# Performance work log

Measured on AMD Instinct MI355X. Metric: run time of the kernel, lower is better.

The kernel has to match this reference:

```python
import jax, jax.numpy as jnp
import numpy as np

B, T, N, H, RC, APT = 8, 32, 144, 16, 16, 10
HN = H * N          # 2304
RCN = RC * N        # 2304
NUM_LAYERS = 2


def _lstm_scan(x, Wih, Whh, bih, bhh):
    # x: [B, D, T] -> hidden states [B, HN, T]; matches torch.nn.LSTMCell math
    b = x.shape[0]
    hd = Whh.shape[1]
    xs = jnp.moveaxis(x, 2, 0)  # [T, B, D]

    def step(carry, xt):
        h, c = carry
        g = xt @ Wih.T + bih + h @ Whh.T + bhh  # [B, 4*HN]
        i, f, gg, o = jnp.split(g, 4, axis=1)
        c = jax.nn.sigmoid(f) * c + jax.nn.sigmoid(i) * jnp.tanh(gg)
        h = jax.nn.sigmoid(o) * jnp.tanh(c)
        return (h, c), h

    init = (jnp.zeros((b, hd), x.dtype), jnp.zeros((b, hd), x.dtype))
    _, hs = jax.lax.scan(step, init, xs)  # [T, B, HN]
    return jnp.moveaxis(hs, 0, 2)  # [B, HN, T]


def _graph_conv(x, A, Wg, bg):
    # x: [B, H, N, T]; diffusion order 2 over one adaptive support, then 1x1 conv
    x1 = jnp.einsum('bcvt,vw->bcwt', x, A)
    x2 = jnp.einsum('bcvt,vw->bcwt', x1, A)
    h = jnp.concatenate([x, x1, x2], axis=1)  # [B, 3H, N, T]
    return jnp.einsum('bcnt,oc->bont', h, Wg) + bg[None, :, None, None]


def _bn(x, g, b, eps=1e-5):
    # BatchNorm2d in training mode (batch statistics over N,H,W)
    m = x.mean(axis=(0, 2, 3), keepdims=True)
    v = x.var(axis=(0, 2, 3), keepdims=True)
    return g[None, :, None, None] * (x - m) * jax.lax.rsqrt(v + eps) + b[None, :, None, None]


def _forward(input_tensor, mask, input_tensor_bw, mask_bw, y, ymask,
             ws, bs, wc, bc, nodevec1, nodevec2,
             Wih_fw, Whh_fw, bih_fw, bhh_fw,
             Wih_bw, Whh_bw, bih_bw, bhh_bw,
             Wg, bg, gamma, beta,
             W_end1, b_end1, W_end2, b_end2,
             W_lo, b_lo, W_f1, b_f1, W_f2, b_f2):

    def feat(inp, m):
        # stack->transpose(2,3) then two 1x1 convs (in_channels=1 each), summed
        f1 = jnp.swapaxes(inp, 1, 2)[:, None]  # [B,1,N,T]
        f2 = jnp.swapaxes(m, 1, 2)[:, None]
        return (ws[None, :, None, None] * f1 + bs[None, :, None, None]
                + wc[None, :, None, None] * f2 + bc[None, :, None, None])

    x = feat(input_tensor, mask)          # [B, RC, N, T]
    x_bw = feat(input_tensor_bw, mask_bw)
    adp = jax.nn.softmax(jax.nn.relu(nodevec1 @ nodevec2), axis=1)  # [N, N]

    outputs = None
    for l in range(NUM_LAYERS):
        t_l = x.shape[3]
        hs = _lstm_scan(x.reshape(B, -1, t_l), Wih_fw[l], Whh_fw[l], bih_fw[l], bhh_fw[l])
        if l == 0:
            hs_bw = _lstm_scan(x_bw.reshape(B, -1, t_l), Wih_bw, Whh_bw, bih_bw, bhh_bw)
            hs = (hs + hs_bw[..., ::-1]) / 2.0
        gcn_in = jnp.tanh(hs.reshape(B, H, N, t_l))
        go = _graph_conv(gcn_in, adp, Wg[l], bg[l])  # [B, RC, N, t_l]
        outputs = go if outputs is None else go + outputs[..., -t_l:]
        x = _bn(go[..., ::2], gamma[l], beta[l])  # halve time dim

    out = jnp.einsum('bcnt,oc->bont', outputs, W_end1) + b_end1[None, :, None, None]
    out = jnp.einsum('bcnt,oc->bont', out, W_end2) + b_end2[None, :, None, None]
    out = jnp.einsum('bcnt,t->bcn', out, W_lo[0]) + b_lo[0]  # linear over time, squeeze
    out = jnp.concatenate([out, y, ymask], axis=-1)  # [B, T, 3N]
    out = out @ W_f1.T + b_f1
    out = out @ W_f2.T + b_f2
    return out  # [B, T, N]


def setup_inputs() -> dict:
    key = jax.random.key(0)
    ks = iter(jax.random.split(key, 48))
    nrm = lambda shape, s=0.05: jax.random.normal(next(ks), shape, dtype=jnp.float32) * s
    rnd = lambda shape: jax.random.uniform(next(ks), shape, dtype=jnp.float32)
    d = {}
    for name in ['input_tensor', 'mask', 'input_tensor_bw', 'mask_bw', 'y', 'ymask']:
        d[name] = rnd((B, T, N))
    d['ws'] = nrm((RC,), 0.2); d['bs'] = nrm((RC,))
    d['wc'] = nrm((RC,), 0.2); d['bc'] = nrm((RC,))
    d['nodevec1'] = nrm((N, APT), 1.0); d['nodevec2'] = nrm((APT, N), 1.0)
    d['Wih_fw'] = nrm((NUM_LAYERS, 4 * HN, RCN), 0.02)
    d['Whh_fw'] = nrm((NUM_LAYERS, 4 * HN, HN), 0.02)
    d['bih_fw'] = nrm((NUM_LAYERS, 4 * HN)); d['bhh_fw'] = nrm((NUM_LAYERS, 4 * HN))
    d['Wih_bw'] = nrm((4 * HN, RCN), 0.02); d['Whh_bw'] = nrm((4 * HN, HN), 0.02)
    d['bih_bw'] = nrm((4 * HN,)); d['bhh_bw'] = nrm((4 * HN,))
    d['Wg'] = nrm((NUM_LAYERS, RC, 3 * H), 0.1); d['bg'] = nrm((NUM_LAYERS, RC))
    d['gamma'] = jnp.ones((NUM_LAYERS, RC), jnp.float32)
    d['beta'] = jnp.zeros((NUM_LAYERS, RC), jnp.float32)
    d['W_end1'] = nrm((H, RC), 0.1); d['b_end1'] = nrm((H,))
    d['W_end2'] = nrm((T, H), 0.1); d['b_end2'] = nrm((T,))
    d['W_lo'] = nrm((1, T // 2), 0.1); d['b_lo'] = nrm((1,))
    d['W_f1'] = nrm((128, 3 * N), 0.05); d['b_f1'] = nrm((128,))
    d['W_f2'] = nrm((N, 128), 0.05); d['b_f2'] = nrm((N,))
    return d


def reference(input_tensor, mask, input_tensor_bw, mask_bw, y, ymask,
              ws, bs, wc, bc, nodevec1, nodevec2,
              Wih_fw, Whh_fw, bih_fw, bhh_fw,
              Wih_bw, Whh_bw, bih_bw, bhh_bw,
              Wg, bg, gamma, beta,
              W_end1, b_end1, W_end2, b_end2,
              W_lo, b_lo, W_f1, b_f1, W_f2, b_f2):
    return _forward(input_tensor, mask, input_tensor_bw, mask_bw, y, ymask,
                    ws, bs, wc, bc, nodevec1, nodevec2,
                    Wih_fw, Whh_fw, bih_fw, bhh_fw,
                    Wih_bw, Whh_bw, bih_bw, bhh_bw,
                    Wg, bg, gamma, beta,
                    W_end1, b_end1, W_end2, b_end2,
                    W_lo, b_lo, W_f1, b_f1, W_f2, b_f2)
```

## Files before the change

### kernel.cpp

```cpp
#include <hip/hip_runtime.h>
#include <cstdint>
#include <cstddef>

#define HN_ 2304
#define G4_ 9216

typedef __attribute__((ext_vector_type(8))) short v8s;
typedef __attribute__((ext_vector_type(4))) float v4f;

__device__ __forceinline__ unsigned short f2bf(float x) {
  union { float f; unsigned int i; } v; v.f = x;
  unsigned int r = (v.i + 0x7fffu + ((v.i >> 16) & 1u)) >> 16;
  return (unsigned short)r;
}

__global__ __launch_bounds__(256) void adp_kernel(const float* __restrict__ nv1,
                                                  const float* __restrict__ nv2,
                                                  float* __restrict__ adp) {
  int i = blockIdx.x;
  int j = threadIdx.x;
  __shared__ float sm[256];
  float r = 0.f, v = -1e30f;
  if (j < 144) {
    for (int k = 0; k < 10; ++k) r += nv1[i * 10 + k] * nv2[k * 144 + j];
    r = fmaxf(r, 0.f);
    v = r;
  }
  sm[j] = v; __syncthreads();
  for (int s = 128; s > 0; s >>= 1) { if (j < s) sm[j] = fmaxf(sm[j], sm[j + s]); __syncthreads(); }
  float mx = sm[0]; __syncthreads();
  float e = (j < 144) ? expf(r - mx) : 0.f;
  sm[j] = e; __syncthreads();
  for (int s = 128; s > 0; s >>= 1) { if (j < s) sm[j] += sm[j + s]; __syncthreads(); }
  float sum = sm[0];
  if (j < 144) adp[i * 144 + j] = e / sum;
}

__global__ __launch_bounds__(256)
void eff_weights(const float* __restrict__ WihF, const float* __restrict__ WihB,
                 const float* __restrict__ bihF, const float* __restrict__ bhhF,
                 const float* __restrict__ bihB, const float* __restrict__ bhhB,
                 const float* __restrict__ ws, const float* __restrict__ bs,
                 const float* __restrict__ wc, const float* __restrict__ bc,
                 unsigned short* __restrict__ Wpk, float* __restrict__ beff) {
  const int r = blockIdx.x, dir = blockIdx.y;
  const float* W = dir ? WihB : WihF;
  __shared__ float red[256];
  const int n = threadIdx.x;
  float spb = 0.f;
  if (n < 144) {
    float sws = 0.f, swc = 0.f;
    #pragma unroll
    for (int c = 0; c < 16; ++c) {
      float w = W[(size_t)r * HN_ + c * 144 + n];
      sws += w * ws[c];
      swc += w * wc[c];
      spb += w * (bs[c] + bc[c]);
    }
    const int rm = r % 2304;
    const int g = r / 2304;
    const int nt = rm >> 2, col = (rm & 3) * 4 + g;
    unsigned short* outp = Wpk + (size_t)dir * 2654208;
    int k = n;
    outp[((size_t)(nt * 9 + (k >> 5)) * 64 + ((k >> 3) & 3) * 16 + col) * 8 + (k & 7)] = f2bf(sws);
    k = 144 + n;
    outp[((size_t)(nt * 9 + (k >> 5)) * 64 + ((k >> 3) & 3) * 16 + col) * 8 + (k & 7)] = f2bf(swc);
  }
  red[n] = spb; __syncthreads();
  for (int s = 128; s > 0; s >>= 1) { if (n < s) red[n] += red[n + s]; __syncthreads(); }
  if (n == 0) {
    const float* bih = dir ? bihB : bihF;
    const float* bhh = dir ? bhhB : bhhF;
    beff[dir * G4_ + r] = red[0] + bih[r] + bhh[r];
  }
}

__global__ void build_acat_frag(const float* __restrict__ inF, const float* __restrict__ mF,
                                const float* __restrict__ inB, const float* __restrict__ mB,
                                unsigned short* __restrict__ out) {
  int idx = blockIdx.x * 256 + threadIdx.x;
  int lane = idx & 63;
  int ks = (idx >> 6) % 9;
  int mt = (idx / (64 * 9)) % 16;
  int dir = idx / (64 * 9 * 16);
  int m = mt * 16 + (lane & 15);
  int k = ks * 32 + (lane >> 4) * 8;
  int t = m >> 3, b = m & 7;
  const float* src; int kk = k;
  if (k < 144) src = dir ? inB : inF;
  else { src = dir ? mB : mF; kk = k - 144; }
  const float* p = src + ((size_t)b * 32 + t) * 144 + kk;
  v8s o;
  #pragma unroll
  for (int e = 0; e < 8; ++e) o[e] = (short)f2bf(p[e]);
  ((v8s*)out)[idx] = o;
}

__global__ void pack_whh(const float* __restrict__ W, unsigned short* __restrict__ out) {
  int idx = blockIdx.x * 256 + threadIdx.x;
  int lane = idx & 63;
  int ks = (idx >> 6) % 72;
  int nt = idx / (64 * 72);
  int col = lane & 15, q = lane >> 4;
  int r = (col & 3) * 2304 + nt * 4 + (col >> 2);
  int k = ks * 32 + q * 8;
  const float* src = W + (size_t)r * 2304 + k;
  float4 v0 = *(const float4*)src;
  float4 v1 = *(const float4*)(src + 4);
  v8s o;
  o[0] = (short)f2bf(v0.x); o[1] = (short)f2bf(v0.y);
  o[2] = (short)f2bf(v0.z); o[3] = (short)f2bf(v0.w);
  o[4] = (short)f2bf(v1.x); o[5] = (short)f2bf(v1.y);
  o[6] = (short)f2bf(v1.z); o[7] = (short)f2bf(v1.w);
  ((v8s*)out)[idx] = o;
}

__global__ __launch_bounds__(64)
void gemm_frag(const unsigned short* __restrict__ Apk, const unsigned short* __restrict__ Wpk,
               const float* __restrict__ b1, const float* __restrict__ b2,
               float* __restrict__ Gx, int nks) {
  const int lane = threadIdx.x;
  const int nt = blockIdx.x;
  const int mtb = blockIdx.y * 4;
  v4f acc[4] = {};
  const v8s* Bp = (const v8s*)Wpk + (size_t)nt * nks * 64;
  const v8s* Ap = (const v8s*)Apk;
  for (int ks = 0; ks < nks; ++ks) {
    v8s bf = Bp[ks * 64 + lane];
    #pragma unroll
    for (int mi = 0; mi < 4; ++mi) {
      v8s af = Ap[(size_t)((mtb + mi) * nks + ks) * 64 + lane];
      acc[mi] = __builtin_amdgcn_mfma_f32_16x16x32_bf16(af, bf, acc[mi], 0, 0, 0);
    }
  }
  const int col = lane & 15;
  const int jj = col >> 2, g = col & 3;
  const int rw = g * 2304 + nt * 4 + jj;
  float bsum = b1[rw] + (b2 ? b2[rw] : 0.f);
  #pragma unroll
  for (int mi = 0; mi < 4; ++mi)
    #pragma unroll
    for (int r = 0; r < 4; ++r) {
      int m = (mtb + mi) * 16 + (lane >> 4) * 4 + r;
      int t = m >> 3, b = m & 7;
      Gx[((size_t)t * 576 + nt) * 128 + col * 8 + b] = acc[mi][r] + bsum;
    }
}

__global__ __launch_bounds__(256)
void lstm_mfma(const unsigned short* __restrict__ Wpk0, const unsigned short* __restrict__ Wpk1,
               const float* __restrict__ Gx0, const float* __restrict__ Gx1,
               const unsigned short* __restrict__ hin0, const unsigned short* __restrict__ hin1,
               unsigned short* __restrict__ hout0, unsigned short* __restrict__ hout1,
               float* __restrict__ c0, float* __restrict__ c1,
               float* __restrict__ hs0, float* __restrict__ hs1,
               int t, int t_l) {
  const int dir = blockIdx.y;
  const unsigned short* Wpk = dir ? Wpk1 : Wpk0;
  const float* Gx = (dir ? Gx1 : Gx0) + (size_t)t * 73728;
  const unsigned short* hin = dir ? hin1 : hin0;
  unsigned short* hout = dir ? hout1 : hout0;
  float* cb = dir ? c1 : c0;
  float* hsout = dir ? hs1 : hs0;

  __shared__ unsigned short Ash[36864];
  for (int i = threadIdx.x; i < 4608; i += 256)
    ((float4*)Ash)[i] = ((const float4*)hin)[i];
  __syncthreads();

  const int lane = threadIdx.x & 63;
  const int wave = threadIdx.x >> 6;
  const int nt = blockIdx.x * 4 + wave;

  v4f acc = {0.f, 0.f, 0.f, 0.f};
  const v8s* Ap = (const v8s*)Ash;
  const v8s* Bp = (const v8s*)Wpk + (size_t)nt * 72 * 64;
  #pragma unroll 8
  for (int ks = 0; ks < 72; ++ks) {
    v8s af = Ap[ks * 64 + lane];
    v8s bf = Bp[ks * 64 + lane];
    acc = __builtin_amdgcn_mfma_f32_16x16x32_bf16(af, bf, acc, 0, 0, 0);
  }

  float vI[4], vF[4], vG[4], vO[4];
  #pragma unroll
  for (int r = 0; r < 4; ++r) {
    float a = acc[r];
    vI[r] = a;
    vF[r] = __shfl_xor(a, 1, 64);
    vG[r] = __shfl_xor(a, 2, 64);
    vO[r] = __shfl_xor(a, 3, 64);
  }
  const int col = lane & 15;
  if ((lane & 3) == 0 && lane < 32) {
    const int j = nt * 4 + (col >> 2);
    #pragma unroll
    for (int r = 0; r < 4; ++r) {
      const int b = (lane >> 4) * 4 + r;
      const float gi = vI[r] + Gx[(nt * 16 + col + 0) * 8 + b];
      const float gf = vF[r] + Gx[(nt * 16 + col + 1) * 8 + b];
      const float gg = vG[r] + Gx[(nt * 16 + col + 2) * 8 + b];
      const float go = vO[r] + Gx[(nt * 16 + col + 3) * 8 + b];
      const float si = 1.f / (1.f + expf(-gi));
      const float sf = 1.f / (1.f + expf(-gf));
      const float so = 1.f / (1.f + expf(-go));
      const float cn = sf * cb[b * HN_ + j] + si * tanhf(gg);
      const float hv = so * tanhf(cn);
      cb[b * HN_ + j] = cn;
      hsout[(size_t)(b * HN_ + j) * t_l + t] = hv;
      hout[((size_t)(j >> 5) * 64 + ((j >> 3) & 3) * 16 + b) * 8 + (j & 7)] = f2bf(hv);
    }
  }
}

__global__ void combine_tanh(const float* __restrict__ hsF, const float* __restrict__ hsB,
                             float* __restrict__ gin, int t_l, int total) {
  int idx = blockIdx.x * 256 + threadIdx.x;
  if (idx >= total) return;
  int t = idx % t_l;
  float v;
  if (hsB) v = 0.5f * (hsF[idx] + hsB[idx - t + (t_l - 1 - t)]);
  else v = hsF[idx];
  gin[idx] = tanhf(v);
}

__global__ void gc1(const float* __restrict__ in, const float* __restrict__ A,
                    float* __restrict__ out, int t_l, int total) {
  int idx = blockIdx.x * 256 + threadIdx.x;
  if (idx >= total) return;
  int t = idx % t_l;
  int w = (idx / t_l) % 144;
  int bc = idx / (t_l * 144);
  const float* src = in + (size_t)bc * 144 * t_l + t;
  float acc = 0.f;
  for (int v = 0; v < 144; ++v) acc += src[(size_t)v * t_l] * A[v * 144 + w];
  out[idx] = acc;
}

__global__ void gc_out(const float* __restrict__ g0, const float* __restrict__ g1,
                       const float* __restrict__ g2, const float* __restrict__ Wg,
                       const float* __restrict__ bg, const float* __restrict__ prev,
                       float* __restrict__ out, int t_l, int total) {
  int idx = blockIdx.x * 256 + threadIdx.x;
  if (idx >= total) return;
  int t = idx % t_l;
  int n = (idx / t_l) % 144;
  int o = (idx / (t_l * 144)) % 16;
  int b = idx / (t_l * 144 * 16);
  float acc = bg[o];
  size_t base = ((size_t)b * 16 * 144 + n) * t_l + t;
  #pragma unroll
  for (int c = 0; c < 16; ++c) {
    size_t s = base + (size_t)c * 144 * t_l;
    acc += Wg[o * 48 + c] * g0[s] + Wg[o * 48 + 16 + c] * g1[s] + Wg[o * 48 + 32 + c] * g2[s];
  }
  if (prev) acc += prev[((size_t)(b * 16 + o) * 144 + n) * 32 + 16 + t];
  out[idx] = acc;
}

__global__ __launch_bounds__(256)
void bn_xt(const float* __restrict__ go, const float* __restrict__ gamma,
           const float* __restrict__ beta, unsigned short* __restrict__ xbf) {
  int c = blockIdx.x;
  __shared__ float s1[256], s2[256];
  float sum = 0.f, sq = 0.f;
  for (int i = threadIdx.x; i < 18432; i += 256) {
    int b = i / 2304; int rem = i - b * 2304; int n = rem / 16; int tt = rem & 15;
    float v = go[((size_t)(b * 16 + c) * 144 + n) * 32 + 2 * tt];
    sum += v; sq += v * v;
  }
  s1[threadIdx.x] = sum; s2[threadIdx.x] = sq; __syncthreads();
  for (int s = 128; s > 0; s >>= 1) {
    if (threadIdx.x < s) { s1[threadIdx.x] += s1[threadIdx.x + s]; s2[threadIdx.x] += s2[threadIdx.x + s]; }
    __syncthreads();
  }
  float mean = s1[0] / 18432.f;
  float var = s2[0] / 18432.f - mean * mean;
  float rs = rsqrtf(var + 1e-5f);
  float scale = gamma[c] * rs, shift = beta[c] - mean * scale;
  for (int i = threadIdx.x; i < 18432; i += 256) {
    int b = i / 2304; int rem = i - b * 2304; int n = rem / 16; int tt = rem & 15;
    float v = go[((size_t)(b * 16 + c) * 144 + n) * 32 + 2 * tt];
    int m = tt * 8 + b;
    int k = c * 144 + n;
    size_t pos = ((size_t)((m >> 4) * 72 + (k >> 5)) * 64 + ((k >> 3) & 3) * 16 + (m & 15)) * 8 + (k & 7);
    xbf[pos] = f2bf(v * scale + shift);
  }
}

__global__ void e1_kernel(const float* __restrict__ in, const float* __restrict__ W,
                          const float* __restrict__ bias, float* __restrict__ out) {
  int idx = blockIdx.x * 256 + threadIdx.x;
  int tt = idx & 15;
  int n = (idx >> 4) % 144;
  int o = (idx / (16 * 144)) % 16;
  int b = idx / (16 * 144 * 16);
  float acc = bias[o];
  size_t base = ((size_t)b * 16 * 144 + n) * 16 + tt;
  #pragma unroll
  for (int c = 0; c < 16; ++c) acc += in[base + (size_t)c * 144 * 16] * W[o * 16 + c];
  out[idx] = acc;
}
__global__ void e2_kernel(const float* __restrict__ in, const float* __restrict__ W,
                          const float* __restrict__ bias, float* __restrict__ out) {
  int idx = blockIdx.x * 256 + threadIdx.x;
  int tt = idx & 15;
  int n = (idx >> 4) % 144;
  int o2 = (idx / (16 * 144)) % 32;
  int b = idx / (16 * 144 * 32);
  float acc = bias[o2];
  size_t base = ((size_t)b * 16 * 144 + n) * 16 + tt;
  #pragma unroll
  for (int o = 0; o < 16; ++o) acc += in[base + (size_t)o * 144 * 16] * W[o2 * 16 + o];
  out[idx] = acc;
}
__global__ void e3_kernel(const float* __restrict__ in, const float* __restrict__ Wlo,
                          const float* __restrict__ blo, float* __restrict__ out) {
  int idx = blockIdx.x * 256 + threadIdx.x;
  int n = idx % 144;
  int o2 = (idx / 144) % 32;
  int b = idx / (144 * 32);
  float acc = blo[0];
  size_t base = ((size_t)(b * 32 + o2) * 144 + n) * 16;
  #pragma unroll
  for (int tt = 0; tt < 16; ++tt) acc += in[base + tt] * Wlo[tt];
  out[idx] = acc;
}
__global__ void f1_kernel(const float* __restrict__ o3, const float* __restrict__ y,
                          const float* __restrict__ ym, const float* __restrict__ W,
                          const float* __restrict__ bias, float* __restrict__ out) {
  int idx = blockIdx.x * 256 + threadIdx.x;
  int k = idx & 127;
  int t = (idx >> 7) & 31;
  int b = idx >> 12;
  float acc = bias[k];
  size_t rb = (size_t)(b * 32 + t) * 144;
  const float* wr = W + k * 432;
  for (int n = 0; n < 144; ++n)
    acc += o3[rb + n] * wr[n] + y[rb + n] * wr[144 + n] + ym[rb + n] * wr[288 + n];
  out[idx] = acc;
}
__global__ void f2_kernel(const float* __restrict__ f1b, const float* __restrict__ W,
                          const float* __restrict__ bias, float* __restrict__ out) {
  int idx = blockIdx.x * 256 + threadIdx.x;
  int n = idx % 144;
  int t = (idx / 144) % 32;
  int b = idx / (144 * 32);
  float acc = bias[n];
  size_t fb = (size_t)(b * 32 + t) * 128;
  const float* wr = W + n * 128;
  #pragma unroll 4
  for (int k = 0; k < 128; ++k) acc += f1b[fb + k] * wr[k];
  out[idx] = acc;
}

extern "C" void kernel_launch(void* const* d_in, const int* in_sizes, int n_in,
                              void* d_out, int out_size, void* d_ws, size_t ws_size,
                              hipStream_t stream) {
  const float* input_tensor = (const float*)d_in[0];
  const float* mask_    = (const float*)d_in[1];
  const float* input_bw = (const float*)d_in[2];
  const float* mask_bw  = (const float*)d_in[3];
  const float* y_in     = (const float*)d_in[4];
  const float* ymask    = (const float*)d_in[5];
  const float* ws_p = (const float*)d_in[6];
  const float* bs_p = (const float*)d_in[7];
  const float* wc_p = (const float*)d_in[8];
  const float* bc_p = (const float*)d_in[9];
  const float* nv1 = (const float*)d_in[10];
  const float* nv2 = (const float*)d_in[11];
  const float* Wih_fw = (const float*)d_in[12];
  const float* Whh_fw = (const float*)d_in[13];
  const float* bih_fw = (const float*)d_in[14];
  const float* bhh_fw = (const float*)d_in[15];
  const float* Wih_bw = (const float*)d_in[16];
  const float* Whh_bw = (const float*)d_in[17];
  const float* bih_bw = (const float*)d_in[18];
  const float* bhh_bw = (const float*)d_in[19];
  const float* Wg   = (const float*)d_in[20];
  const float* bg   = (const float*)d_in[21];
  const float* gam  = (const float*)d_in[22];
  const float* bet  = (const float*)d_in[23];
  const float* W_end1 = (const float*)d_in[24];
  const float* b_end1 = (const float*)d_in[25];
  const float* W_end2 = (const float*)d_in[26];
  const float* b_end2 = (const float*)d_in[27];
  const float* W_lo = (const float*)d_in[28];
  const float* b_lo = (const float*)d_in[29];
  const float* W_f1 = (const float*)d_in[30];
  const float* b_f1 = (const float*)d_in[31];
  const float* W_f2 = (const float*)d_in[32];
  const float* b_f2 = (const float*)d_in[33];

  char* base = (char*)d_ws;
  size_t off = 0;
  auto alloc = [&](size_t bytes) -> char* {
    char* p = base + off;
    off += (bytes + 255) & ~(size_t)255;
    return p;
  };
  float* adp   = (float*)alloc(144 * 144 * 4);
  unsigned short* Weffpk = (unsigned short*)alloc((size_t)2 * 2654208 * 2);
  float* beff  = (float*)alloc(2 * G4_ * 4);
  unsigned short* acatf  = (unsigned short*)alloc((size_t)2 * 73728 * 2);
  float* GxF   = (float*)alloc((size_t)32 * 73728 * 4);
  float* GxB   = (float*)alloc((size_t)32 * 73728 * 4);
  char*  zreg  = alloc(6 * 147456 + 3 * 73728);
  float* hsF   = (float*)alloc((size_t)589824 * 4);
  float* hsB   = (float*)alloc((size_t)589824 * 4);
  float* hsL   = (float*)alloc((size_t)294912 * 4);
  float* gin   = (float*)alloc((size_t)589824 * 4);
  float* x1b   = (float*)alloc((size_t)589824 * 4);
  float* x2b   = (float*)alloc((size_t)589824 * 4);
  float* out0  = (float*)alloc((size_t)589824 * 4);
  float* out1  = (float*)alloc((size_t)294912 * 4);
  unsigned short* xbf = (unsigned short*)alloc((size_t)294912 * 2);
  float* tmp1  = (float*)alloc((size_t)294912 * 4);
  float* tmp2  = (float*)alloc((size_t)589824 * 4);
  float* out3  = (float*)alloc((size_t)36864 * 4);
  float* f1b   = (float*)alloc((size_t)32768 * 4);
  unsigned short* P0 = (unsigned short*)alloc((size_t)2654208 * 8 * 2);
  unsigned short* P1 = (unsigned short*)alloc((size_t)2654208 * 8 * 2);

  unsigned short* hbfF[2] = {(unsigned short*)zreg, (unsigned short*)(zreg + 147456)};
  unsigned short* hbfB[2] = {(unsigned short*)(zreg + 2 * 147456), (unsigned short*)(zreg + 3 * 147456)};
  unsigned short* hbfL[2] = {(unsigned short*)(zreg + 4 * 147456), (unsigned short*)(zreg + 5 * 147456)};
  float* cF = (float*)(zreg + 6 * 147456);
  float* cB = (float*)(zreg + 6 * 147456 + 73728);
  float* cL = (float*)(zreg + 6 * 147456 + 2 * 73728);

  hipMemsetAsync(zreg, 0, 6 * 147456 + 3 * 73728, stream);

  adp_kernel<<<144, 256, 0, stream>>>(nv1, nv2, adp);
  eff_weights<<<dim3(G4_, 2), 256, 0, stream>>>(Wih_fw, Wih_bw, bih_fw, bhh_fw, bih_bw, bhh_bw,
                                                ws_p, bs_p, wc_p, bc_p, Weffpk, beff);
  build_acat_frag<<<72, 256, 0, stream>>>(input_tensor, mask_, input_bw, mask_bw, acatf);
  gemm_frag<<<dim3(576, 4), 64, 0, stream>>>(acatf, Weffpk, beff, nullptr, GxF, 9);
  gemm_frag<<<dim3(576, 4), 64, 0, stream>>>(acatf + 73728, Weffpk + 2654208, beff + G4_, nullptr, GxB, 9);
  pack_whh<<<10368, 256, 0, stream>>>(Whh_fw, P0);
  pack_whh<<<10368, 256, 0, stream>>>(Whh_bw, P1);

  for (int t = 0; t < 32; ++t) {
    lstm_mfma<<<dim3(144, 2), 256, 0, stream>>>(
        P0, P1, GxF, GxB,
        hbfF[t & 1], hbfB[t & 1], hbfF[(t + 1) & 1], hbfB[(t + 1) & 1],
        cF, cB, hsF, hsB, t, 32);
  }

  combine_tanh<<<2304, 256, 0, stream>>>(hsF, hsB, gin, 32, 589824);
  gc1<<<2304, 256, 0, stream>>>(gin, adp, x1b, 32, 589824);
  gc1<<<2304, 256, 0, stream>>>(x1b, adp, x2b, 32, 589824);
  gc_out<<<2304, 256, 0, stream>>>(gin, x1b, x2b, Wg, bg, nullptr, out0, 32, 589824);
  bn_xt<<<16, 256, 0, stream>>>(out0, gam, bet, xbf);

  const size_t WL1_off = (size_t)G4_ * HN_;
  pack_whh<<<10368, 256, 0, stream>>>(Wih_fw + WL1_off, P1);
  gemm_frag<<<dim3(576, 2), 64, 0, stream>>>(xbf, P1, bih_fw + G4_, bhh_fw + G4_, GxF, 72);
  pack_whh<<<10368, 256, 0, stream>>>(Whh_fw + WL1_off, P0);

  for (int t = 0; t < 16; ++t) {
    lstm_mfma<<<dim3(144, 1), 256, 0, stream>>>(
        P0, P0, GxF, GxF,
        hbfL[t & 1], hbfL[t & 1], hbfL[(t + 1) & 1], hbfL[(t + 1) & 1],
        cL, cL, hsL, hsL, t, 16);
  }

  combine_tanh<<<1152, 256, 0, stream>>>(hsL, nullptr, gin, 16, 294912);
  gc1<<<1152, 256, 0, stream>>>(gin, adp, x1b, 16, 294912);
  gc1<<<1152, 256, 0, stream>>>(x1b, adp, x2b, 16, 294912);
  gc_out<<<1152, 256, 0, stream>>>(gin, x1b, x2b, Wg + 16 * 48, bg + 16, out0, out1, 16, 294912);

  e1_kernel<<<1152, 256, 0, stream>>>(out1, W_end1, b_end1, tmp1);
  e2_kernel<<<2304, 256, 0, stream>>>(tmp1, W_end2, b_end2, tmp2);
  e3_kernel<<<144, 256, 0, stream>>>(tmp2, W_lo, b_lo, out3);
  f1_kernel<<<128, 256, 0, stream>>>(out3, y_in, ymask, W_f1, b_f1, f1b);
  f2_kernel<<<144, 256, 0, stream>>>(f1b, W_f2, b_f2, (float*)d_out);
}
```

Measured before the change: 1.745 ms.

## Replace per-timestep LSTM launches with persistent cooperative scan kernel

```diff
diff --git a/kernel.cpp b/kernel.cpp
--- a/kernel.cpp
+++ b/kernel.cpp
@@ -1,6 +1,9 @@
 #include <hip/hip_runtime.h>
+#include <hip/hip_cooperative_groups.h>
 #include <cstdint>
 #include <cstddef>
+
+namespace cg = cooperative_groups;
 
 #define HN_ 2304
 #define G4_ 9216
@@ -147,69 +150,102 @@
     }
 }
 
-__global__ __launch_bounds__(256)
-void lstm_mfma(const unsigned short* __restrict__ Wpk0, const unsigned short* __restrict__ Wpk1,
+__global__ __launch_bounds__(256, 2)
+void lstm_scan(const unsigned short* __restrict__ Wpk0, const unsigned short* __restrict__ Wpk1,
                const float* __restrict__ Gx0, const float* __restrict__ Gx1,
-               const unsigned short* __restrict__ hin0, const unsigned short* __restrict__ hin1,
-               unsigned short* __restrict__ hout0, unsigned short* __restrict__ hout1,
-               float* __restrict__ c0, float* __restrict__ c1,
+               unsigned short* hbuf,
                float* __restrict__ hs0, float* __restrict__ hs1,
-               int t, int t_l) {
-  const int dir = blockIdx.y;
-  const unsigned short* Wpk = dir ? Wpk1 : Wpk0;
-  const float* Gx = (dir ? Gx1 : Gx0) + (size_t)t * 73728;
-  const unsigned short* hin = dir ? hin1 : hin0;
-  unsigned short* hout = dir ? hout1 : hout0;
-  float* cb = dir ? c1 : c0;
-  float* hsout = dir ? hs1 : hs0;
-
-  __shared__ unsigned short Ash[36864];
-  for (int i = threadIdx.x; i < 4608; i += 256)
-    ((float4*)Ash)[i] = ((const float4*)hin)[i];
-  __syncthreads();
+               int T, int blocksPerDir) {
+  cg::grid_group grid = cg::this_grid();
+  const int dir = blockIdx.x / blocksPerDir;
+  const int cidx = blockIdx.x - dir * blocksPerDir;
+  const unsigned short* __restrict__ Wpk = dir ? Wpk1 : Wpk0;
+  const float* __restrict__ Gxb = dir ? Gx1 : Gx0;
+  float* __restrict__ hsout = dir ? hs1 : hs0;
+  unsigned short* hb = hbuf + (size_t)dir * 2 * 18432;
 
   const int lane = threadIdx.x & 63;
   const int wave = threadIdx.x >> 6;
-  const int nt = blockIdx.x * 4 + wave;
-
-  v4f acc = {0.f, 0.f, 0.f, 0.f};
-  const v8s* Ap = (const v8s*)Ash;
-  const v8s* Bp = (const v8s*)Wpk + (size_t)nt * 72 * 64;
-  #pragma unroll 8
-  for (int ks = 0; ks < 72; ++ks) {
-    v8s af = Ap[ks * 64 + lane];
-    v8s bf = Bp[ks * 64 + lane];
-    acc = __builtin_amdgcn_mfma_f32_16x16x32_bf16(af, bf, acc, 0, 0, 0);
-  }
-
-  float vI[4], vF[4], vG[4], vO[4];
-  #pragma unroll
-  for (int r = 0; r < 4; ++r) {
-    float a = acc[r];
-    vI[r] = a;
-    vF[r] = __shfl_xor(a, 1, 64);
-    vG[r] = __shfl_xor(a, 2, 64);
-    vO[r] = __shfl_xor(a, 3, 64);
-  }
+  const int nt = cidx * 4 + wave;
+
+  __shared__ __align__(16) unsigned short Ash[18432];
+
+  const v8s* __restrict__ Bs = (const v8s*)Wpk + (size_t)nt * 72 * 64 + lane;
+
+  v8s wreg[36];
+  #pragma unroll
+  for (int k = 0; k < 36; ++k) wreg[k] = Bs[k * 64];
+
+  const int afoff = (lane >> 4) * 8 + (lane & 7);
   const int col = lane & 15;
-  if ((lane & 3) == 0 && lane < 32) {
-    const int j = nt * 4 + (col >> 2);
+  const int j = nt * 4 + (col >> 2);
+  const int brow = (lane >> 4) * 4;
+  const bool act = ((lane & 3) == 0) && (lane < 32);
+  float creg[4] = {0.f, 0.f, 0.f, 0.f};
+
+  for (int t = 0; t < T; ++t) {
+    const unsigned short* hcur = hb + (t & 1) * 18432;
+    unsigned short* hnxt = hb + ((t + 1) & 1) * 18432;
+
+    for (int i = threadIdx.x; i < 2304; i += 256)
+      ((float4*)Ash)[i] = ((const float4*)hcur)[i];
+    __syncthreads();
+
+    const v8s* Ap = (const v8s*)Ash;
+    v4f acc0 = {0.f, 0.f, 0.f, 0.f}, acc1 = {0.f, 0.f, 0.f, 0.f};
+
+    v8s bf[6], nb[6];
+    #pragma unroll
+    for (int u = 0; u < 6; ++u) bf[u] = Bs[(36 + u) * 64];
+
+    #pragma unroll
+    for (int k = 0; k < 36; ++k) {
+      v8s af = Ap[k * 32 + afoff];
+      acc0 = __builtin_amdgcn_mfma_f32_16x16x32_bf16(af, wreg[k], acc0, 0, 0, 0);
+    }
+    #pragma unroll
+    for (int c = 0; c < 6; ++c) {
+      #pragma unroll
+      for (int u = 0; u < 6; ++u) { if (c < 5) nb[u] = Bs[(42 + c * 6 + u) * 64]; }
+      #pragma unroll
+      for (int u = 0; u < 6; ++u) {
+        v8s af = Ap[(36 + c * 6 + u) * 32 + afoff];
+        acc1 = __builtin_amdgcn_mfma_f32_16x16x32_bf16(af, bf[u], acc1, 0, 0, 0);
+      }
+      #pragma unroll
+      for (int u = 0; u < 6; ++u) { if (c < 5) bf[u] = nb[u]; }
+    }
+
+    float vI[4], vF[4], vG[4], vO[4];
     #pragma unroll
     for (int r = 0; r < 4; ++r) {
-      const int b = (lane >> 4) * 4 + r;
-      const float gi = vI[r] + Gx[(nt * 16 + col + 0) * 8 + b];
-      const float gf = vF[r] + Gx[(nt * 16 + col + 1) * 8 + b];
-      const float gg = vG[r] + Gx[(nt * 16 + col + 2) * 8 + b];
-      const float go = vO[r] + Gx[(nt * 16 + col + 3) * 8 + b];
-      const float si = 1.f / (1.f + expf(-gi));
-      const float sf = 1.f / (1.f + expf(-gf));
-      const float so = 1.f / (1.f + expf(-go));
-      const float cn = sf * cb[b * HN_ + j] + si * tanhf(gg);
-      const float hv = so * tanhf(cn);
-      cb[b * HN_ + j] = cn;
-      hsout[(size_t)(b * HN_ + j) * t_l + t] = hv;
-      hout[((size_t)(j >> 5) * 64 + ((j >> 3) & 3) * 16 + b) * 8 + (j & 7)] = f2bf(hv);
-    }
+      float a = acc0[r] + acc1[r];
+      vI[r] = a;
+      vF[r] = __shfl_xor(a, 1, 64);
+      vG[r] = __shfl_xor(a, 2, 64);
+      vO[r] = __shfl_xor(a, 3, 64);
+    }
+    if (act) {
+      const float* Gx = Gxb + (size_t)t * 73728 + (size_t)(nt * 16 + col) * 8;
+      #pragma unroll
+      for (int r = 0; r < 4; ++r) {
+        const int b = brow + r;
+        const float gi = vI[r] + Gx[b];
+        const float gf = vF[r] + Gx[8 + b];
+        const float gg = vG[r] + Gx[16 + b];
+        const float go = vO[r] + Gx[24 + b];
+        const float si = 1.f / (1.f + expf(-gi));
+        const float sf = 1.f / (1.f + expf(-gf));
+        const float so = 1.f / (1.f + expf(-go));
+        const float cn = sf * creg[r] + si * tanhf(gg);
+        creg[r] = cn;
+        const float hv = so * tanhf(cn);
+        hsout[(size_t)(b * HN_ + j) * T + t] = hv;
+        hnxt[((j >> 5) * 32 + ((j >> 3) & 3) * 8 + b) * 8 + (j & 7)] = f2bf(hv);
+      }
+    }
+    __threadfence();
+    grid.sync();
   }
 }
 
@@ -405,7 +441,7 @@
   unsigned short* acatf  = (unsigned short*)alloc((size_t)2 * 73728 * 2);
   float* GxF   = (float*)alloc((size_t)32 * 73728 * 4);
   float* GxB   = (float*)alloc((size_t)32 * 73728 * 4);
-  char*  zreg  = alloc(6 * 147456 + 3 * 73728);
+  char*  hz    = alloc(147456 + 73728);
   float* hsF   = (float*)alloc((size_t)589824 * 4);
   float* hsB   = (float*)alloc((size_t)589824 * 4);
   float* hsL   = (float*)alloc((size_t)294912 * 4);
@@ -422,14 +458,10 @@
   unsigned short* P0 = (unsigned short*)alloc((size_t)2654208 * 8 * 2);
   unsigned short* P1 = (unsigned short*)alloc((size_t)2654208 * 8 * 2);
 
-  unsigned short* hbfF[2] = {(unsigned short*)zreg, (unsigned short*)(zreg + 147456)};
-  unsigned short* hbfB[2] = {(unsigned short*)(zreg + 2 * 147456), (unsigned short*)(zreg + 3 * 147456)};
-  unsigned short* hbfL[2] = {(unsigned short*)(zreg + 4 * 147456), (unsigned short*)(zreg + 5 * 147456)};
-  float* cF = (float*)(zreg + 6 * 147456);
-  float* cB = (float*)(zreg + 6 * 147456 + 73728);
-  float* cL = (float*)(zreg + 6 * 147456 + 2 * 73728);
-
-  hipMemsetAsync(zreg, 0, 6 * 147456 + 3 * 73728, stream);
+  unsigned short* hbuf0 = (unsigned short*)hz;
+  unsigned short* hbufL = (unsigned short*)(hz + 147456);
+
+  hipMemsetAsync(hz, 0, 147456 + 73728, stream);
 
   adp_kernel<<<144, 256, 0, stream>>>(nv1, nv2, adp);
   eff_weights<<<dim3(G4_, 2), 256, 0, stream>>>(Wih_fw, Wih_bw, bih_fw, bhh_fw, bih_bw, bhh_bw,
@@ -440,11 +472,14 @@
   pack_whh<<<10368, 256, 0, stream>>>(Whh_fw, P0);
   pack_whh<<<10368, 256, 0, stream>>>(Whh_bw, P1);
 
-  for (int t = 0; t < 32; ++t) {
-    lstm_mfma<<<dim3(144, 2), 256, 0, stream>>>(
-        P0, P1, GxF, GxB,
-        hbfF[t & 1], hbfB[t & 1], hbfF[(t + 1) & 1], hbfB[(t + 1) & 1],
-        cF, cB, hsF, hsB, t, 32);
+  {
+    const unsigned short* aW0 = P0; const unsigned short* aW1 = P1;
+    const float* aG0 = GxF; const float* aG1 = GxB;
+    unsigned short* ah = hbuf0;
+    float* ahs0 = hsF; float* ahs1 = hsB;
+    int aT = 32, aB = 144;
+    void* args[] = {&aW0, &aW1, &aG0, &aG1, &ah, &ahs0, &ahs1, &aT, &aB};
+    hipLaunchCooperativeKernel((void*)lstm_scan, dim3(288), dim3(256), args, 0, stream);
   }
 
   combine_tanh<<<2304, 256, 0, stream>>>(hsF, hsB, gin, 32, 589824);
@@ -458,11 +493,14 @@
   gemm_frag<<<dim3(576, 2), 64, 0, stream>>>(xbf, P1, bih_fw + G4_, bhh_fw + G4_, GxF, 72);
   pack_whh<<<10368, 256, 0, stream>>>(Whh_fw + WL1_off, P0);
 
-  for (int t = 0; t < 16; ++t) {
-    lstm_mfma<<<dim3(144, 1), 256, 0, stream>>>(
-        P0, P0, GxF, GxF,
-        hbfL[t & 1], hbfL[t & 1], hbfL[(t + 1) & 1], hbfL[(t + 1) & 1],
-        cL, cL, hsL, hsL, t, 16);
+  {
+    const unsigned short* aW0 = P0; const unsigned short* aW1 = P0;
+    const float* aG0 = GxF; const float* aG1 = GxF;
+    unsigned short* ah = hbufL;
+    float* ahs0 = hsL; float* ahs1 = hsL;
+    int aT = 16, aB = 144;
+    void* args[] = {&aW0, &aW1, &aG0, &aG1, &ah, &ahs0, &ahs1, &aT, &aB};
+    hipLaunchCooperativeKernel((void*)lstm_scan, dim3(144), dim3(256), args, 0, stream);
   }
 
   combine_tanh<<<1152, 256, 0, stream>>>(hsL, nullptr, gin, 16, 294912);
```

Result: slower. 3.874 ms (+122.0%).

## Split LSTM step K-reduction across waves and compact h layout to drop padding

Applied to the files above, without the earlier changes.

```diff
diff --git a/kernel.cpp b/kernel.cpp
--- a/kernel.cpp
+++ b/kernel.cpp
@@ -147,68 +147,76 @@
     }
 }
 
-__global__ __launch_bounds__(256)
-void lstm_mfma(const unsigned short* __restrict__ Wpk0, const unsigned short* __restrict__ Wpk1,
+__global__ __launch_bounds__(256, 4)
+void lstm_step(const unsigned short* __restrict__ Wpk0, const unsigned short* __restrict__ Wpk1,
                const float* __restrict__ Gx0, const float* __restrict__ Gx1,
                const unsigned short* __restrict__ hin0, const unsigned short* __restrict__ hin1,
                unsigned short* __restrict__ hout0, unsigned short* __restrict__ hout1,
                float* __restrict__ c0, float* __restrict__ c1,
                float* __restrict__ hs0, float* __restrict__ hs1,
-               int t, int t_l) {
+               int t, int T) {
   const int dir = blockIdx.y;
-  const unsigned short* Wpk = dir ? Wpk1 : Wpk0;
-  const float* Gx = (dir ? Gx1 : Gx0) + (size_t)t * 73728;
-  const unsigned short* hin = dir ? hin1 : hin0;
-  unsigned short* hout = dir ? hout1 : hout0;
-  float* cb = dir ? c1 : c0;
-  float* hsout = dir ? hs1 : hs0;
-
-  __shared__ unsigned short Ash[36864];
-  for (int i = threadIdx.x; i < 4608; i += 256)
-    ((float4*)Ash)[i] = ((const float4*)hin)[i];
-  __syncthreads();
+  const unsigned short* __restrict__ Wpk = dir ? Wpk1 : Wpk0;
+  const float* __restrict__ Gxb = dir ? Gx1 : Gx0;
+  const unsigned short* __restrict__ hin = dir ? hin1 : hin0;
+  unsigned short* __restrict__ hout = dir ? hout1 : hout0;
+  float* __restrict__ cb = dir ? c1 : c0;
+  float* __restrict__ hsout = dir ? hs1 : hs0;
 
   const int lane = threadIdx.x & 63;
   const int wave = threadIdx.x >> 6;
-  const int nt = blockIdx.x * 4 + wave;
+  const int nt = blockIdx.x;
+
+  const int afoff = (lane >> 4) * 8 + (lane & 7);
+  const v8s* __restrict__ Aq = (const v8s*)hin + (size_t)(wave * 18) * 32 + afoff;
+  const v8s* __restrict__ Bq = (const v8s*)Wpk + (size_t)nt * 72 * 64 + (size_t)(wave * 18) * 64 + lane;
 
   v4f acc = {0.f, 0.f, 0.f, 0.f};
-  const v8s* Ap = (const v8s*)Ash;
-  const v8s* Bp = (const v8s*)Wpk + (size_t)nt * 72 * 64;
-  #pragma unroll 8
-  for (int ks = 0; ks < 72; ++ks) {
-    v8s af = Ap[ks * 64 + lane];
-    v8s bf = Bp[ks * 64 + lane];
+  #pragma unroll
+  for (int k = 0; k < 18; ++k) {
+    v8s af = Aq[k * 32];
+    v8s bf = Bq[k * 64];
     acc = __builtin_amdgcn_mfma_f32_16x16x32_bf16(af, bf, acc, 0, 0, 0);
   }
 
-  float vI[4], vF[4], vG[4], vO[4];
-  #pragma unroll
-  for (int r = 0; r < 4; ++r) {
-    float a = acc[r];
-    vI[r] = a;
-    vF[r] = __shfl_xor(a, 1, 64);
-    vG[r] = __shfl_xor(a, 2, 64);
-    vO[r] = __shfl_xor(a, 3, 64);
-  }
-  const int col = lane & 15;
-  if ((lane & 3) == 0 && lane < 32) {
-    const int j = nt * 4 + (col >> 2);
+  __shared__ v4f red[3][64];
+  if (wave) red[wave - 1][lane] = acc;
+  __syncthreads();
+  if (wave == 0) {
+    acc += red[0][lane];
+    acc += red[1][lane];
+    acc += red[2][lane];
+
+    float vI[4], vF[4], vG[4], vO[4];
     #pragma unroll
     for (int r = 0; r < 4; ++r) {
-      const int b = (lane >> 4) * 4 + r;
-      const float gi = vI[r] + Gx[(nt * 16 + col + 0) * 8 + b];
-      const float gf = vF[r] + Gx[(nt * 16 + col + 1) * 8 + b];
-      const float gg = vG[r] + Gx[(nt * 16 + col + 2) * 8 + b];
-      const float go = vO[r] + Gx[(nt * 16 + col + 3) * 8 + b];
-      const float si = 1.f / (1.f + expf(-gi));
-      const float sf = 1.f / (1.f + expf(-gf));
-      const float so = 1.f / (1.f + expf(-go));
-      const float cn = sf * cb[b * HN_ + j] + si * tanhf(gg);
-      const float hv = so * tanhf(cn);
-      cb[b * HN_ + j] = cn;
-      hsout[(size_t)(b * HN_ + j) * t_l + t] = hv;
-      hout[((size_t)(j >> 5) * 64 + ((j >> 3) & 3) * 16 + b) * 8 + (j & 7)] = f2bf(hv);
+      float a = acc[r];
+      vI[r] = a;
+      vF[r] = __shfl_xor(a, 1, 64);
+      vG[r] = __shfl_xor(a, 2, 64);
+      vO[r] = __shfl_xor(a, 3, 64);
+    }
+    const int col = lane & 15;
+    if ((lane & 3) == 0 && lane < 32) {
+      const int j = nt * 4 + (col >> 2);
+      const int brow = (lane >> 4) * 4;
+      const float* Gx = Gxb + (size_t)t * 73728 + (size_t)(nt * 16 + col) * 8;
+      #pragma unroll
+      for (int r = 0; r < 4; ++r) {
+        const int b = brow + r;
+        const float gi = vI[r] + Gx[b];
+        const float gf = vF[r] + Gx[8 + b];
+        const float gg = vG[r] + Gx[16 + b];
+        const float go = vO[r] + Gx[24 + b];
+        const float si = 1.f / (1.f + expf(-gi));
+        const float sf = 1.f / (1.f + expf(-gf));
+        const float so = 1.f / (1.f + expf(-go));
+        const float cn = sf * cb[b * HN_ + j] + si * tanhf(gg);
+        cb[b * HN_ + j] = cn;
+        const float hv = so * tanhf(cn);
+        hsout[(size_t)(b * HN_ + j) * T + t] = hv;
+        hout[((j >> 5) * 32 + ((j >> 3) & 3) * 8 + b) * 8 + (j & 7)] = f2bf(hv);
+      }
     }
   }
 }
@@ -405,7 +413,7 @@
   unsigned short* acatf  = (unsigned short*)alloc((size_t)2 * 73728 * 2);
   float* GxF   = (float*)alloc((size_t)32 * 73728 * 4);
   float* GxB   = (float*)alloc((size_t)32 * 73728 * 4);
-  char*  zreg  = alloc(6 * 147456 + 3 * 73728);
+  char*  hz    = alloc(442368);
   float* hsF   = (float*)alloc((size_t)589824 * 4);
   float* hsB   = (float*)alloc((size_t)589824 * 4);
   float* hsL   = (float*)alloc((size_t)294912 * 4);
@@ -422,14 +430,14 @@
   unsigned short* P0 = (unsigned short*)alloc((size_t)2654208 * 8 * 2);
   unsigned short* P1 = (unsigned short*)alloc((size_t)2654208 * 8 * 2);
 
-  unsigned short* hbfF[2] = {(unsigned short*)zreg, (unsigned short*)(zreg + 147456)};
-  unsigned short* hbfB[2] = {(unsigned short*)(zreg + 2 * 147456), (unsigned short*)(zreg + 3 * 147456)};
-  unsigned short* hbfL[2] = {(unsigned short*)(zreg + 4 * 147456), (unsigned short*)(zreg + 5 * 147456)};
-  float* cF = (float*)(zreg + 6 * 147456);
-  float* cB = (float*)(zreg + 6 * 147456 + 73728);
-  float* cL = (float*)(zreg + 6 * 147456 + 2 * 73728);
-
-  hipMemsetAsync(zreg, 0, 6 * 147456 + 3 * 73728, stream);
+  unsigned short* hF[2] = {(unsigned short*)hz,            (unsigned short*)(hz + 36864)};
+  unsigned short* hB[2] = {(unsigned short*)(hz + 73728),  (unsigned short*)(hz + 110592)};
+  unsigned short* hL[2] = {(unsigned short*)(hz + 147456), (unsigned short*)(hz + 184320)};
+  float* cF = (float*)(hz + 221184);
+  float* cB = (float*)(hz + 294912);
+  float* cL = (float*)(hz + 368640);
+
+  hipMemsetAsync(hz, 0, 442368, stream);
 
   adp_kernel<<<144, 256, 0, stream>>>(nv1, nv2, adp);
   eff_weights<<<dim3(G4_, 2), 256, 0, stream>>>(Wih_fw, Wih_bw, bih_fw, bhh_fw, bih_bw, bhh_bw,
@@ -441,9 +449,9 @@
   pack_whh<<<10368, 256, 0, stream>>>(Whh_bw, P1);
 
   for (int t = 0; t < 32; ++t) {
-    lstm_mfma<<<dim3(144, 2), 256, 0, stream>>>(
+    lstm_step<<<dim3(576, 2), 256, 0, stream>>>(
         P0, P1, GxF, GxB,
-        hbfF[t & 1], hbfB[t & 1], hbfF[(t + 1) & 1], hbfB[(t + 1) & 1],
+        hF[t & 1], hB[t & 1], hF[(t + 1) & 1], hB[(t + 1) & 1],
         cF, cB, hsF, hsB, t, 32);
   }
 
@@ -459,9 +467,9 @@
   pack_whh<<<10368, 256, 0, stream>>>(Whh_fw + WL1_off, P0);
 
   for (int t = 0; t < 16; ++t) {
-    lstm_mfma<<<dim3(144, 1), 256, 0, stream>>>(
+    lstm_step<<<dim3(576, 1), 256, 0, stream>>>(
         P0, P0, GxF, GxF,
-        hbfL[t & 1], hbfL[t & 1], hbfL[(t + 1) & 1], hbfL[(t + 1) & 1],
+        hL[t & 1], hL[t & 1], hL[(t + 1) & 1], hL[(t + 1) & 1],
         cL, cL, hsL, hsL, t, 16);
   }
 
```

After: 1.487 ms. -14.8%, faster.
